# Performance work log

Hardware: AMD Instinct MI355X
Metric: run time of the kernel (lower is better)

The kernel has to match this reference:

```python
import jax, jax.numpy as jnp
import numpy as np

NUM_HEADS = 16
EPS = 1e-6


def _phi(x):
    # Positive feature map: ELU + 1
    return jax.nn.elu(x) + 1.0


def setup_inputs() -> dict:
    key = jax.random.key(0)
    ks = jax.random.split(key, 5)
    B, L, D = 4, 8192, 1024
    scale = 0.02
    return {
        "x": jax.random.normal(ks[0], (B, L, D), dtype=jnp.float32),
        "Wq": jax.random.normal(ks[1], (D, D), dtype=jnp.float32) * scale,
        "Wk": jax.random.normal(ks[2], (D, D), dtype=jnp.float32) * scale,
        "Wv": jax.random.normal(ks[3], (D, D), dtype=jnp.float32) * scale,
        "Wo": jax.random.normal(ks[4], (D, D), dtype=jnp.float32) * scale,
    }


def reference(x, Wq, Wk, Wv, Wo):
    B, L, D = x.shape
    H = NUM_HEADS
    dh = D // H
    # Projections (bias-free linear layers)
    Q = x @ Wq
    K = x @ Wk
    V = x @ Wv
    # Split heads: (B, H, L, dh)
    Qh = Q.reshape(B, L, H, dh).transpose(0, 2, 1, 3)
    Kh = K.reshape(B, L, H, dh).transpose(0, 2, 1, 3)
    Vh = V.reshape(B, L, H, dh).transpose(0, 2, 1, 3)
    Qf = _phi(Qh)
    Kf = _phi(Kh)
    # Global key-value reduction over time: (B, H, dh, dh)
    Kv = jnp.einsum('bhlm,bhln->bhmn', Kf, Vh)
    # Key normalizer: (B, H, dh)
    K1 = jnp.sum(Kf, axis=2)
    # Numerator / denominator
    num = jnp.einsum('bhlm,bhmn->bhln', Qf, Kv)
    den = jnp.einsum('bhlm,bhm->bhl', Qf, K1) + EPS
    out = num / den[..., None]
    out = out.transpose(0, 2, 1, 3).reshape(B, L, D)
    return out @ Wo
```

## Files before the change

### kernel.cpp

```cpp
#include <hip/hip_runtime.h>
#include <stdint.h>
#include <stddef.h>

typedef __bf16 bf16;
typedef __attribute__((ext_vector_type(8))) __bf16 bf16x8;
typedef __attribute__((ext_vector_type(4))) __bf16 bf16x4;
typedef __attribute__((ext_vector_type(4))) float f32x4;

#define ATT_EPS 1e-6f

__device__ __forceinline__ void lds16(const void* g, void* l) {
    __builtin_amdgcn_global_load_lds(
        (const __attribute__((address_space(1))) void*)g,
        (__attribute__((address_space(3))) void*)l, 16, 0, 0);
}

__global__ __launch_bounds__(256) void cvt_bf16(const float4* __restrict__ in,
                                                bf16x4* __restrict__ out, int n4) {
    int i = blockIdx.x * 256 + threadIdx.x;
    if (i < n4) {
        float4 v = in[i];
        bf16x4 o;
        o.x = (bf16)v.x; o.y = (bf16)v.y; o.z = (bf16)v.z; o.w = (bf16)v.w;
        out[i] = o;
    }
}

__global__ __launch_bounds__(256) void transpose_w(const float* __restrict__ W,
                                                   bf16* __restrict__ Wt) {
    __shared__ float tile[32][33];
    const int bx = blockIdx.x * 32, by = blockIdx.y * 32;
    const int tx = threadIdx.x, ty = threadIdx.y;
#pragma unroll
    for (int j = 0; j < 32; j += 8)
        tile[ty + j][tx] = W[(size_t)(by + ty + j) * 1024 + bx + tx];
    __syncthreads();
#pragma unroll
    for (int j = 0; j < 32; j += 8)
        Wt[(size_t)(bx + ty + j) * 1024 + by + tx] = (bf16)tile[tx][ty + j];
}

template <int MODE>
__global__ __launch_bounds__(512) void gemm256(const bf16* __restrict__ A, int lda,
                                               const bf16* __restrict__ B, int ldb,
                                               void* __restrict__ C, int ldc,
                                               int K, int fast_m, int fl2) {
    __shared__ bf16 smem[65536] __attribute__((aligned(16)));
    const int t = threadIdx.x;
    const int wave = t >> 6, lane = t & 63;
    const int q8 = gridDim.x >> 3;
    const int wg = (blockIdx.x & 7) * q8 + (blockIdx.x >> 3);
    const int f = wg & ((1 << fl2) - 1), s = wg >> fl2;
    const int mt = fast_m ? f : s, nt = fast_m ? s : f;
    const int tileM = mt << 8, tileN = nt << 8;
    const int wm = wave >> 2, wn = wave & 3;

    int rowS[2], colS[2];
#pragma unroll
    for (int j = 0; j < 2; j++) {
        int off = t * 16 + j * 8192;
        int o = off & 1023;
        int op = o ^ (((o >> 9) & 1) << 5);
        rowS[j] = (off >> 10) * 16 + (op >> 6);
        colS[j] = (op & 63) >> 1;
    }
    const int rm = lane & 15, qq = lane >> 4;
    const int foff = ((rm * 64 + qq * 16) ^ ((rm >> 3) << 5)) >> 1;

    f32x4 acc[8][4] = {};

#define STAGE(tt)                                                              \
    {                                                                          \
        bf16* sA_ = smem + ((tt) & 3) * 16384;                                 \
        bf16* sB_ = sA_ + 8192;                                                \
        const int k0_ = (tt) << 5;                                             \
        _Pragma("unroll") for (int j = 0; j < 2; j++) {                        \
            lds16(A + (size_t)(tileM + rowS[j]) * lda + k0_ + colS[j],         \
                  sA_ + wave * 512 + j * 4096);                                \
            lds16(B + (size_t)(tileN + rowS[j]) * ldb + k0_ + colS[j],         \
                  sB_ + wave * 512 + j * 4096);                                \
        }                                                                      \
    }

#define COMPUTE(tt)                                                            \
    {                                                                          \
        const bf16* pA_ = smem + ((tt) & 3) * 16384 + wm * 4096 + foff;        \
        const bf16* pB_ = smem + ((tt) & 3) * 16384 + 8192 + wn * 2048 + foff; \
        bf16x8 af_[8], bv_[4];                                                 \
        _Pragma("unroll") for (int mi = 0; mi < 8; mi++)                       \
            af_[mi] = *(const bf16x8*)(pA_ + mi * 512);                        \
        _Pragma("unroll") for (int ni = 0; ni < 4; ni++)                       \
            bv_[ni] = *(const bf16x8*)(pB_ + ni * 512);                        \
        __builtin_amdgcn_s_setprio(1);                                         \
        _Pragma("unroll") for (int mi = 0; mi < 8; mi++)                       \
            _Pragma("unroll") for (int ni = 0; ni < 4; ni++)                   \
                acc[mi][ni] = __builtin_amdgcn_mfma_f32_16x16x32_bf16(         \
                    af_[mi], bv_[ni], acc[mi][ni], 0, 0, 0);                   \
        __builtin_amdgcn_s_setprio(0);                                         \
    }

#define SYNCV(n)                                                               \
    asm volatile("s_waitcnt vmcnt(" #n ")" ::: "memory");                      \
    __builtin_amdgcn_s_barrier();                                              \
    __builtin_amdgcn_sched_barrier(0);

    const int NT = K >> 5;
    STAGE(0); STAGE(1); STAGE(2);
    SYNCV(8);
    for (int tt = 0; tt < NT - 3; ++tt) {
        STAGE(tt + 3);
        COMPUTE(tt);
        SYNCV(8);
    }
    COMPUTE(NT - 3); SYNCV(4);
    COMPUTE(NT - 2); SYNCV(0);
    COMPUTE(NT - 1);
#undef STAGE
#undef COMPUTE
#undef SYNCV

    const int row0 = (lane >> 4) * 4, col = lane & 15;
    if (MODE == 0) {
        float* Cf = (float*)C;
#pragma unroll
        for (int mi = 0; mi < 8; mi++)
#pragma unroll
            for (int ni = 0; ni < 4; ni++)
#pragma unroll
                for (int r = 0; r < 4; r++) {
                    int gm = tileM + wm * 128 + mi * 16 + row0 + r;
                    int gn = tileN + wn * 64 + ni * 16 + col;
                    Cf[(size_t)gm * ldc + gn] = acc[mi][ni][r];
                }
    } else {
        __syncthreads();
        bf16* Cb = (bf16*)C;
#pragma unroll
        for (int mi = 0; mi < 8; mi++)
#pragma unroll
            for (int ni = 0; ni < 4; ni++)
#pragma unroll
                for (int r = 0; r < 4; r++) {
                    float v = acc[mi][ni][r];
                    if (MODE == 2) v = (v > 0.f) ? (v + 1.f) : __expf(v);
                    smem[(wm * 128 + mi * 16 + row0 + r) * 256 +
                         wn * 64 + ni * 16 + col] = (bf16)v;
                }
        __syncthreads();
#pragma unroll
        for (int i = 0; i < 16; i++) {
            int c = t + i * 512;
            int row = c >> 5, cb = (c & 31) * 8;
            *(bf16x8*)&Cb[(size_t)(tileM + row) * ldc + tileN + cb] =
                *(const bf16x8*)&smem[row * 256 + cb];
        }
    }
}

__global__ __launch_bounds__(256) void kv_reduce(const bf16* __restrict__ Kft,
                                                 const bf16* __restrict__ Vt,
                                                 float* __restrict__ Kv) {
    const int chunk = blockIdx.x;
    const int bh = blockIdx.y;
    const int b = bh >> 4, h = bh & 15;
    __shared__ bf16 sA[64 * 32] __attribute__((aligned(16)));
    __shared__ bf16 sB[64 * 32] __attribute__((aligned(16)));
    const int t = threadIdx.x, wave = t >> 6, lane = t & 63;
    const size_t cbase = (size_t)b * 8192 + (size_t)chunk * 1024;
    const int srow = t >> 2, scol = (t & 3) * 8;
    const bf16* a0 = Kft + (size_t)(h * 64 + srow) * 32768 + cbase + scol;
    const bf16* b0 = Vt + (size_t)(h * 64 + srow) * 32768 + cbase + scol;
    bf16* dA = sA + wave * 512;
    bf16* dB = sB + wave * 512;
    const int rm = lane & 15, qk = (lane >> 4) * 8;

    f32x4 acc[4] = {};
    f32x4 acc1 = {0.f, 0.f, 0.f, 0.f};
    bf16x8 ones;
#pragma unroll
    for (int j = 0; j < 8; j++) ones[j] = (bf16)1.0f;

    for (int k0 = 0; k0 < 1024; k0 += 32) {
        lds16(a0 + k0, dA);
        lds16(b0 + k0, dB);
        __builtin_amdgcn_s_waitcnt(0);
        __syncthreads();
        bf16x8 af = *(const bf16x8*)&sA[(wave * 16 + rm) * 32 + qk];
        bf16x8 bfr[4];
#pragma unroll
        for (int ni = 0; ni < 4; ni++)
            bfr[ni] = *(const bf16x8*)&sB[(ni * 16 + rm) * 32 + qk];
#pragma unroll
        for (int ni = 0; ni < 4; ni++)
            acc[ni] = __builtin_amdgcn_mfma_f32_16x16x32_bf16(af, bfr[ni], acc[ni], 0, 0, 0);
        acc1 = __builtin_amdgcn_mfma_f32_16x16x32_bf16(af, ones, acc1, 0, 0, 0);
        __syncthreads();
    }

    float* out = Kv + bh * 65 * 64;
    const int row0 = (lane >> 4) * 4, col = lane & 15;
    const int m0 = wave * 16 + row0;
#pragma unroll
    for (int ni = 0; ni < 4; ni++)
#pragma unroll
        for (int r = 0; r < 4; r++)
            atomicAdd(&out[(ni * 16 + col) * 64 + m0 + r], acc[ni][r]);
    if (col == 0) {
#pragma unroll
        for (int r = 0; r < 4; r++) atomicAdd(&out[64 * 64 + m0 + r], acc1[r]);
    }
}

__global__ __launch_bounds__(256) void attn_out(const bf16* __restrict__ Qf,
                                                const float* __restrict__ Kv,
                                                bf16* __restrict__ attn) {
    const int lt = blockIdx.x;
    const int bh = blockIdx.y;
    const int b = bh >> 4, h = bh & 15;
    constexpr int EP_STRIDE = 80;
    __shared__ bf16 smem[13312] __attribute__((aligned(16)));
    __shared__ float den[128];
    bf16* sQ = smem;
    bf16* sB = smem + 8192;
    const int t = threadIdx.x, wave = t >> 6, lane = t & 63;
    const int qrow = t >> 3, qc = (t & 7) * 8;
    const bf16* qp = Qf + (size_t)(b * 8192 + lt * 128 + qrow) * 1024 + h * 64 + qc;
#pragma unroll
    for (int i = 0; i < 4; i++)
        lds16(qp + (size_t)i * 32 * 1024, sQ + i * 2048 + wave * 512);
    const float* kv = Kv + bh * 65 * 64;
    for (int idx = t; idx < 80 * 64; idx += 256) {
        int n = idx >> 6, k2 = idx & 63;
        sB[idx] = (n < 65) ? (bf16)kv[n * 64 + k2] : (bf16)0.f;
    }
    __builtin_amdgcn_s_waitcnt(0);
    __syncthreads();

    f32x4 acc[2][5] = {};
    const int rm = lane & 15, qk = (lane >> 4) * 8;
#pragma unroll
    for (int k0 = 0; k0 < 64; k0 += 32) {
        bf16x8 af[2], bfr[5];
#pragma unroll
        for (int mi = 0; mi < 2; mi++)
            af[mi] = *(const bf16x8*)&sQ[(wave * 32 + mi * 16 + rm) * 64 + k0 + qk];
#pragma unroll
        for (int ni = 0; ni < 5; ni++)
            bfr[ni] = *(const bf16x8*)&sB[(ni * 16 + rm) * 64 + k0 + qk];
#pragma unroll
        for (int mi = 0; mi < 2; mi++)
#pragma unroll
            for (int ni = 0; ni < 5; ni++)
                acc[mi][ni] = __builtin_amdgcn_mfma_f32_16x16x32_bf16(
                    af[mi], bfr[ni], acc[mi][ni], 0, 0, 0);
    }

    const int row0 = (lane >> 4) * 4, col = lane & 15;
    if (col == 0) {
#pragma unroll
        for (int mi = 0; mi < 2; mi++)
#pragma unroll
            for (int r = 0; r < 4; r++)
                den[wave * 32 + mi * 16 + row0 + r] = acc[mi][4][r] + ATT_EPS;
    }
    __syncthreads();
#pragma unroll
    for (int mi = 0; mi < 2; mi++)
#pragma unroll
        for (int ni = 0; ni < 4; ni++)
#pragma unroll
            for (int r = 0; r < 4; r++) {
                int rl = wave * 32 + mi * 16 + row0 + r;
                smem[rl * EP_STRIDE + ni * 16 + col] =
                    (bf16)(acc[mi][ni][r] / den[rl]);
            }
    __syncthreads();
    const int er = t >> 3, ec = (t & 7) * 8;
#pragma unroll
    for (int i = 0; i < 4; i++) {
        int row = er + i * 32;
        *(bf16x8*)&attn[(size_t)(b * 8192 + lt * 128 + row) * 1024 + h * 64 + ec] =
            *(const bf16x8*)&smem[row * EP_STRIDE + ec];
    }
}

extern "C" void kernel_launch(void* const* d_in, const int* in_sizes, int n_in,
                              void* d_out, int out_size, void* d_ws, size_t ws_size,
                              hipStream_t stream) {
    const float* x  = (const float*)d_in[0];
    const float* Wq = (const float*)d_in[1];
    const float* Wk = (const float*)d_in[2];
    const float* Wv = (const float*)d_in[3];
    const float* Wo = (const float*)d_in[4];

    char* ws = (char*)d_ws;
    bf16* xb  = (bf16*)ws;
    bf16* Qf  = (bf16*)(ws + ((size_t)64 << 20));
    bf16* Kft = (bf16*)(ws + ((size_t)128 << 20));
    bf16* Vt  = (bf16*)(ws + ((size_t)192 << 20));
    bf16* Wqt = (bf16*)(ws + ((size_t)256 << 20));
    bf16* Wkt = Wqt + 1024 * 1024;
    bf16* Wvt = Wkt + 1024 * 1024;
    bf16* Wot = Wvt + 1024 * 1024;
    float* Kv = (float*)(Wot + 1024 * 1024);
    bf16* attn = xb;

    cvt_bf16<<<8388608 / 256, 256, 0, stream>>>((const float4*)x, (bf16x4*)xb, 8388608);
    dim3 tb(32, 8);
    transpose_w<<<dim3(32, 32), tb, 0, stream>>>(Wq, Wqt);
    transpose_w<<<dim3(32, 32), tb, 0, stream>>>(Wk, Wkt);
    transpose_w<<<dim3(32, 32), tb, 0, stream>>>(Wv, Wvt);
    transpose_w<<<dim3(32, 32), tb, 0, stream>>>(Wo, Wot);
    hipMemsetAsync(Kv, 0, (size_t)64 * 65 * 64 * sizeof(float), stream);

    gemm256<2><<<512, 512, 0, stream>>>(xb, 1024, Wqt, 1024, Qf, 1024, 1024, 0, 2);
    gemm256<2><<<512, 512, 0, stream>>>(Wkt, 1024, xb, 1024, Kft, 32768, 1024, 1, 2);
    gemm256<1><<<512, 512, 0, stream>>>(Wvt, 1024, xb, 1024, Vt, 32768, 1024, 1, 2);
    kv_reduce<<<dim3(8, 64), 256, 0, stream>>>(Kft, Vt, Kv);
    attn_out<<<dim3(64, 64), 256, 0, stream>>>(Qf, Kv, attn);
    gemm256<0><<<512, 512, 0, stream>>>(attn, 1024, Wot, 1024, d_out, 1024, 1024, 0, 2);
}
```

Baseline: 635.2 us.

## Restructure GEMM main loop to issue LDS reads before stage loads and barrier

Reorganizes the 4-stage GEMM pipeline so each phase first reads its fragments from LDS, then issues the next tile's global->LDS loads, waits on vmcnt, barriers, and only then runs the MFMAs, followed by a second barrier. Global pointers are precomputed outside the loop to cut address arithmetic per stage. The aim is to overlap LDS reads with global load issue and barrier waiting, at the cost of an extra barrier per iteration. The epilogue __syncthreads is dropped because the last phase now ends with a barrier.

```diff
diff --git a/kernel.cpp b/kernel.cpp
--- a/kernel.cpp
+++ b/kernel.cpp
@@ -67,22 +67,24 @@
     const int rm = lane & 15, qq = lane >> 4;
     const int foff = ((rm * 64 + qq * 16) ^ ((rm >> 3) << 5)) >> 1;
 
+    const bf16* gA0 = A + (size_t)(tileM + rowS[0]) * lda + colS[0];
+    const bf16* gA1 = A + (size_t)(tileM + rowS[1]) * lda + colS[1];
+    const bf16* gB0 = B + (size_t)(tileN + rowS[0]) * ldb + colS[0];
+    const bf16* gB1 = B + (size_t)(tileN + rowS[1]) * ldb + colS[1];
+
     f32x4 acc[8][4] = {};
 
 #define STAGE(tt)                                                              \
     {                                                                          \
-        bf16* sA_ = smem + ((tt) & 3) * 16384;                                 \
-        bf16* sB_ = sA_ + 8192;                                                \
+        bf16* base_ = smem + ((tt) & 3) * 16384;                               \
         const int k0_ = (tt) << 5;                                             \
-        _Pragma("unroll") for (int j = 0; j < 2; j++) {                        \
-            lds16(A + (size_t)(tileM + rowS[j]) * lda + k0_ + colS[j],         \
-                  sA_ + wave * 512 + j * 4096);                                \
-            lds16(B + (size_t)(tileN + rowS[j]) * ldb + k0_ + colS[j],         \
-                  sB_ + wave * 512 + j * 4096);                                \
-        }                                                                      \
-    }
-
-#define COMPUTE(tt)                                                            \
+        lds16(gA0 + k0_, base_ + wave * 512);                                  \
+        lds16(gA1 + k0_, base_ + 4096 + wave * 512);                           \
+        lds16(gB0 + k0_, base_ + 8192 + wave * 512);                           \
+        lds16(gB1 + k0_, base_ + 12288 + wave * 512);                          \
+    }
+
+#define PHASE(tt, DOSTG, VM)                                                   \
     {                                                                          \
         const bf16* pA_ = smem + ((tt) & 3) * 16384 + wm * 4096 + foff;        \
         const bf16* pB_ = smem + ((tt) & 3) * 16384 + 8192 + wn * 2048 + foff; \
@@ -91,33 +93,30 @@
             af_[mi] = *(const bf16x8*)(pA_ + mi * 512);                        \
         _Pragma("unroll") for (int ni = 0; ni < 4; ni++)                       \
             bv_[ni] = *(const bf16x8*)(pB_ + ni * 512);                        \
+        if (DOSTG) STAGE((tt) + 3);                                            \
+        asm volatile("s_waitcnt vmcnt(" #VM ")" ::: "memory");                 \
+        __builtin_amdgcn_s_barrier();                                          \
+        asm volatile("s_waitcnt lgkmcnt(0)" ::: "memory");                     \
         __builtin_amdgcn_s_setprio(1);                                         \
         _Pragma("unroll") for (int mi = 0; mi < 8; mi++)                       \
             _Pragma("unroll") for (int ni = 0; ni < 4; ni++)                   \
                 acc[mi][ni] = __builtin_amdgcn_mfma_f32_16x16x32_bf16(         \
                     af_[mi], bv_[ni], acc[mi][ni], 0, 0, 0);                   \
         __builtin_amdgcn_s_setprio(0);                                         \
-    }
-
-#define SYNCV(n)                                                               \
-    asm volatile("s_waitcnt vmcnt(" #n ")" ::: "memory");                      \
-    __builtin_amdgcn_s_barrier();                                              \
-    __builtin_amdgcn_sched_barrier(0);
+        __builtin_amdgcn_s_barrier();                                          \
+    }
 
     const int NT = K >> 5;
     STAGE(0); STAGE(1); STAGE(2);
-    SYNCV(8);
-    for (int tt = 0; tt < NT - 3; ++tt) {
-        STAGE(tt + 3);
-        COMPUTE(tt);
-        SYNCV(8);
-    }
-    COMPUTE(NT - 3); SYNCV(4);
-    COMPUTE(NT - 2); SYNCV(0);
-    COMPUTE(NT - 1);
+    asm volatile("s_waitcnt vmcnt(8)" ::: "memory");
+    __builtin_amdgcn_s_barrier();
+    for (int tt = 0; tt < NT - 3; ++tt)
+        PHASE(tt, 1, 8);
+    PHASE(NT - 3, 0, 4);
+    PHASE(NT - 2, 0, 0);
+    PHASE(NT - 1, 0, 0);
 #undef STAGE
-#undef COMPUTE
-#undef SYNCV
+#undef PHASE
 
     const int row0 = (lane >> 4) * 4, col = lane & 15;
     if (MODE == 0) {
@@ -133,7 +132,6 @@
                     Cf[(size_t)gm * ldc + gn] = acc[mi][ni][r];
                 }
     } else {
-        __syncthreads();
         bf16* Cb = (bf16*)C;
 #pragma unroll
         for (int mi = 0; mi < 8; mi++)
```

After: 653.5 us. 1.03x slower.
